# Performance work log

Measured on AMD Instinct MI355X. Metric: run time of the kernel, lower is better.

The kernel has to match this reference:

```python
import jax, jax.numpy as jnp
import numpy as np

BRANCH = 8
LEVELS = 7
N = (BRANCH ** LEVELS - 1) // (BRANCH - 1)  # 299593 nodes, complete 8-ary tree
VOCAB, IN_DIM, MEM = 50000, 300, 150


def _tree_structure():
    parent = np.empty(N, np.int32)
    parent[0] = N  # sentinel: root scatters into dropped segment N
    idx = np.arange(1, N)
    parent[1:] = (idx - 1) // BRANCH
    depth = np.empty(N, np.int32)
    start = 0
    for d in range(LEVELS):
        cnt = BRANCH ** d
        depth[start:start + cnt] = d
        start += cnt
    return jnp.asarray(parent), jnp.asarray(depth)


def setup_inputs() -> dict:
    key = jax.random.key(0)
    ks = jax.random.split(key, 20)
    parent, depth = _tree_structure()
    inp = {
        'tokens': jax.random.randint(ks[0], (N,), 0, VOCAB, dtype=jnp.int32),
        'parent': parent,
        'depth': depth,
        'max_depth': LEVELS,
        'emb': jax.random.normal(ks[1], (VOCAB, IN_DIM), jnp.float32) * 0.1,
    }
    names_x = ['Wix', 'Wfx', 'Wox', 'Wux']
    names_h = ['Wih', 'Wfh', 'Woh', 'Wuh']
    sx = 1.0 / np.sqrt(IN_DIM)
    sh = 1.0 / np.sqrt(MEM)
    for j, (nx, nh) in enumerate(zip(names_x, names_h)):
        inp[nx] = jax.random.normal(ks[2 + 4 * j], (MEM, IN_DIM), jnp.float32) * sx
        inp['b' + nx[1:]] = jax.random.normal(ks[3 + 4 * j], (MEM,), jnp.float32) * sx
        inp[nh] = jax.random.normal(ks[4 + 4 * j], (MEM, MEM), jnp.float32) * sh
        inp['b' + nh[1:]] = jax.random.normal(ks[5 + 4 * j], (MEM,), jnp.float32) * sh
    return inp


def reference(tokens, parent, depth, max_depth, emb,
              Wix, bix, Wih, bih, Wfx, bfx, Wfh, bfh,
              Wox, box, Woh, boh, Wux, bux, Wuh, buh):
    n = tokens.shape[0]
    x = emb[tokens]  # [N, in_dim]
    # precompute all input-side gate projections once (batched GEMMs)
    ix_x = x @ Wix.T + bix
    fx_x = x @ Wfx.T + bfx
    ox_x = x @ Wox.T + box
    ux_x = x @ Wux.T + bux
    # parent index safe for gathering (root's sentinel -> 0; its row is masked out)
    gparent = jnp.where(parent >= n, 0, parent)

    h = jnp.zeros((n, MEM), x.dtype)
    c = jnp.zeros((n, MEM), x.dtype)

    # level-synchronous bottom-up sweep (loop over tree depth, not data)
    for d in range(max_depth - 1, -1, -1):
        # per-child forget gate: sigmoid(fh(h_child) + fx(x_parent)) * c_child
        f = jax.nn.sigmoid(h @ Wfh.T + bfh + fx_x[gparent])
        fc_sum = jax.ops.segment_sum(f * c, parent, num_segments=n + 1)[:n]
        h_sum = jax.ops.segment_sum(h, parent, num_segments=n + 1)[:n]
        i = jax.nn.sigmoid(ix_x + h_sum @ Wih.T + bih)
        o = jax.nn.sigmoid(ox_x + h_sum @ Woh.T + boh)
        u = jnp.tanh(ux_x + h_sum @ Wuh.T + buh)
        c_new = i * u + fc_sum
        h_new = o * jnp.tanh(c_new)
        mask = (depth == d)[:, None]
        c = jnp.where(mask, c_new, c)
        h = jnp.where(mask, h_new, h)
    # original returns concatenated cell states (post-order); here indexed by node id
    return c
```

## Files before the change

kernel.cpp:

```cpp
#include <hip/hip_runtime.h>


#define MEMD  150
#define IND   300
#define NINT  37449
#define VOCAB 50000
#define XROW  608
#define FSTR  152
#define NVB   1563
#define NNB   1171

typedef short bf16x8 __attribute__((ext_vector_type(8)));
typedef float f32x16 __attribute__((ext_vector_type(16)));
#define ZERO16 {0,0,0,0,0,0,0,0,0,0,0,0,0,0,0,0}

#define XINT_OFF 0ul
#define HLF_OFF  45540000ul
#define FHX_OFF  60740000ul
#define HSB_OFF  68340000ul
#define FCS_OFF  79730000ul
#define BPX_OFF  91120000ul
#define BPH_OFF  91510000ul

#define CLF_OUT_OFF 0ul

__device__ __forceinline__ float b2f(unsigned short u) {
    union { unsigned int i; float f; } v; v.i = ((unsigned int)u) << 16; return v.f;
}
__device__ __forceinline__ unsigned short f2b(float f) {
    union { float f; unsigned int i; } v; v.f = f;
    unsigned int x = v.i;
    x += 0x7fffu + ((x >> 16) & 1u);
    return (unsigned short)(x >> 16);
}
__device__ __forceinline__ float sigm(float x) {
    return __builtin_amdgcn_rcpf(1.0f + __expf(-x));
}
__device__ __forceinline__ float tanh_fast(float x) {
    float e = __expf(2.0f * x);
    return 1.0f - 2.0f * __builtin_amdgcn_rcpf(e + 1.0f);
}
__device__ __forceinline__ unsigned char f2e4m3(float f) {
    union { float f; unsigned u; } v; v.f = f;
    unsigned s = (v.u >> 31) << 7;
    float af = fabsf(f);
    if (af >= 448.f) return (unsigned char)(s | 0x7E);
    if (af < 0.015625f) {
        int m = (int)(af * 512.f + 0.5f);
        if (m > 7) m = 7;
        return (unsigned char)(s | m);
    }
    unsigned u = v.u & 0x7fffffffu;
    u += 0x7ffffu + ((u >> 20) & 1u);
    int ef = (int)(u >> 23) - 120;
    unsigned m = (u >> 20) & 7u;
    if (ef < 1) { ef = 1; m = 0; }
    if (ef > 15) { ef = 15; m = 6; }
    return (unsigned char)(s | (ef << 3) | m);
}
__device__ __forceinline__ float e4m3f(unsigned char u) {
    unsigned s = (u >> 7) & 1u, ef = (u >> 3) & 15u, m = u & 7u;
    if (ef == 0) {
        float r = (float)m * 0.001953125f;
        return s ? -r : r;
    }
    union { unsigned u; float f; } v;
    v.u = (s << 31) | ((ef + 120) << 23) | (m << 20);
    return v.f;
}

__global__ void pack_w(const float* __restrict__ Wix, const float* __restrict__ Wox,
                       const float* __restrict__ Wux, const float* __restrict__ Wfx,
                       const float* __restrict__ Wih, const float* __restrict__ Woh,
                       const float* __restrict__ Wuh, const float* __restrict__ Wfh,
                       unsigned short* __restrict__ bpx, unsigned short* __restrict__ bph)
{
    const int total_x = 4 * 5 * 19 * 512;
    const int total_h = 4 * 5 * 10 * 512;
    for (int i = blockIdx.x * blockDim.x + threadIdx.x; i < total_x + total_h;
         i += gridDim.x * blockDim.x) {
        if (i < total_x) {
            int e = i & 7, lane = (i >> 3) & 63, rest = i >> 9;
            int ks = rest % 19; rest /= 19;
            int nt = rest % 5;  int g = rest / 5;
            int col = nt * 32 + (lane & 31);
            int k = ks * 16 + ((lane >> 5) << 3) + e;
            const float* W = (g == 0) ? Wix : (g == 1) ? Wox : (g == 2) ? Wux : Wfx;
            bpx[i] = f2b((col < MEMD && k < IND) ? W[col * IND + k] : 0.f);
        } else {
            int j = i - total_x;
            int e = j & 7, lane = (j >> 3) & 63, rest = j >> 9;
            int ks = rest % 10; rest /= 10;
            int nt = rest % 5;  int g = rest / 5;
            int col = nt * 32 + (lane & 31);
            int k = ks * 16 + ((lane >> 5) << 3) + e;
            const float* W = (g == 0) ? Wih : (g == 1) ? Woh : (g == 2) ? Wuh : Wfh;
            bph[j] = f2b((col < MEMD && k < MEMD) ? W[col * MEMD + k] : 0.f);
        }
    }
}

__global__ __launch_bounds__(320, 3)
void xgemm_all(const int* __restrict__ tokens, const float* __restrict__ emb,
               const float* __restrict__ bix, const float* __restrict__ bih,
               const float* __restrict__ box_, const float* __restrict__ boh,
               const float* __restrict__ bux, const float* __restrict__ buh,
               const float* __restrict__ bfx, const float* __restrict__ bfh,
               const unsigned short* __restrict__ bpx_u,
               const unsigned short* __restrict__ bph_u,
               unsigned short* __restrict__ cleaf,
               unsigned short* __restrict__ hleaf,
               unsigned char* __restrict__ fhx,
               unsigned short* __restrict__ xint)
{
    __shared__ __align__(16) char sm0[32768];
    __shared__ int toksL[32];
    const int tid = threadIdx.x, lane = tid & 63, w = tid >> 6;
    const int hi = lane >> 5, ln31 = lane & 31;
    const bool isV = blockIdx.x < NVB;
    const int tile0 = (isV ? blockIdx.x : (blockIdx.x - NVB)) * 32;
    const int rowsValid = min(32, (isV ? VOCAB : NINT) - tile0);

    if (tid < 32) {
        int rr = (tid < rowsValid) ? tid : 0;
        toksL[tid] = isV ? (tile0 + rr) : tokens[tile0 + rr];
    }
    __syncthreads();
    for (int i = tid; i < 32 * 40; i += 320) {
        int r = i / 40, q = i % 40;
        const float* er = emb + (long)toksL[r] * IND;
        float4 v0 = {0.f,0.f,0.f,0.f}, v1 = {0.f,0.f,0.f,0.f};
        if (q < 38) v0 = *(const float4*)(er + q * 8);
        if (q < 37) v1 = *(const float4*)(er + q * 8 + 4);
        bf16x8 p;
        p[0]=(short)f2b(v0.x); p[1]=(short)f2b(v0.y); p[2]=(short)f2b(v0.z); p[3]=(short)f2b(v0.w);
        p[4]=(short)f2b(v1.x); p[5]=(short)f2b(v1.y); p[6]=(short)f2b(v1.z); p[7]=(short)f2b(v1.w);
        *(bf16x8*)(sm0 + r * 640 + ((q * 16) ^ ((r & 7) << 4))) = p;
    }
    __syncthreads();

    const bf16x8* BX = (const bf16x8*)bpx_u;
    const bf16x8* BH = (const bf16x8*)bph_u;
    const int row = ln31, nt = w;
    const int col = nt * 32 + ln31;
    const bool colv = col < MEMD;
    const int cc = colv ? col : 0;

    f32x16 a0 = ZERO16, a1 = ZERO16, a2 = ZERO16, a3 = ZERO16;
    {
        bf16x8 aC = *(const bf16x8*)(sm0 + row * 640 + ((hi * 16) ^ ((row & 7) << 4)));
        bf16x8 b0C = BX[((0 * 5 + nt) * 19 + 0) * 64 + lane];
        bf16x8 b1C = BX[((1 * 5 + nt) * 19 + 0) * 64 + lane];
        bf16x8 b2C = BX[((2 * 5 + nt) * 19 + 0) * 64 + lane];
        bf16x8 b3C = BX[((3 * 5 + nt) * 19 + 0) * 64 + lane];
        #pragma unroll
        for (int ks = 0; ks < 19; ++ks) {
            bf16x8 aN, b0N, b1N, b2N, b3N;
            if (ks < 18) {
                aN  = *(const bf16x8*)(sm0 + row * 640 + (((ks + 1) * 32 + hi * 16) ^ ((row & 7) << 4)));
                b0N = BX[((0 * 5 + nt) * 19 + ks + 1) * 64 + lane];
                b1N = BX[((1 * 5 + nt) * 19 + ks + 1) * 64 + lane];
                b2N = BX[((2 * 5 + nt) * 19 + ks + 1) * 64 + lane];
                if (!isV) b3N = BX[((3 * 5 + nt) * 19 + ks + 1) * 64 + lane];
            }
            a0 = __builtin_amdgcn_mfma_f32_32x32x16_bf16(aC, b0C, a0, 0, 0, 0);
            a1 = __builtin_amdgcn_mfma_f32_32x32x16_bf16(aC, b1C, a1, 0, 0, 0);
            a2 = __builtin_amdgcn_mfma_f32_32x32x16_bf16(aC, b2C, a2, 0, 0, 0);
            if (!isV) a3 = __builtin_amdgcn_mfma_f32_32x32x16_bf16(aC, b3C, a3, 0, 0, 0);
            aC = aN; b0C = b0N; b1C = b1N; b2C = b2N; b3C = b3N;
        }
    }
    const float bi = bix[cc] + bih[cc];
    const float bo = box_[cc] + boh[cc];
    const float bu = bux[cc] + buh[cc];

    if (isV) {
        #pragma unroll
        for (int r = 0; r < 16; ++r) {
            int rloc = (r & 3) + 8 * (r >> 2) + 4 * hi;
            float iv = sigm(a0[r] + bi);
            float ov = sigm(a1[r] + bo);
            float uv = tanh_fast(a2[r] + bu);
            float cv = iv * uv;
            float hv = ov * tanh_fast(cv);
            if (rloc < rowsValid && colv) {
                long o = (long)(tile0 + rloc) * FSTR + col;
                cleaf[o] = f2b(cv);
                hleaf[o] = f2b(hv);
            }
            *(unsigned short*)(sm0 + 20480 + rloc * 384 + ((col * 2) ^ ((rloc & 7) << 4))) = f2b(hv);
        }
        __syncthreads();
        f32x16 ff = ZERO16;
        {
            const char* hb = sm0 + 20480;
            bf16x8 aC = *(const bf16x8*)(hb + row * 384 + ((hi * 16) ^ ((row & 7) << 4)));
            bf16x8 bC = BH[((15 + nt) * 10 + 0) * 64 + lane];
            #pragma unroll
            for (int ks = 0; ks < 10; ++ks) {
                bf16x8 aN, bN;
                if (ks < 9) {
                    aN = *(const bf16x8*)(hb + row * 384 + (((ks + 1) * 32 + hi * 16) ^ ((row & 7) << 4)));
                    bN = BH[((15 + nt) * 10 + ks + 1) * 64 + lane];
                }
                ff = __builtin_amdgcn_mfma_f32_32x32x16_bf16(aC, bC, ff, 0, 0, 0);
                aC = aN; bC = bN;
            }
        }
        if (colv) {
            #pragma unroll
            for (int r = 0; r < 16; ++r) {
                int rloc = (r & 3) + 8 * (r >> 2) + 4 * hi;
                if (rloc < rowsValid)
                    fhx[(long)(tile0 + rloc) * FSTR + col] = f2e4m3(ff[r]);
            }
        }
    } else {
        const float bf = bfx[cc] + bfh[cc];
        #pragma unroll
        for (int r = 0; r < 16; ++r) {
            int rloc = (r & 3) + 8 * (r >> 2) + 4 * hi;
            if (rloc < rowsValid && colv) {
                ushort4 gv;
                gv.x = f2b(a0[r] + bi);
                gv.y = f2b(a1[r] + bo);
                gv.z = f2b(a2[r] + bu);
                gv.w = f2b(a3[r] + bf);
                *(ushort4*)(xint + (long)(tile0 + rloc) * XROW + col * 4) = gv;
            }
        }
    }
}

__global__ __launch_bounds__(320, 8)
void leaf_csum(const int* __restrict__ tokens,
               const unsigned short* __restrict__ cleafU,
               const unsigned short* __restrict__ hleaf,
               const unsigned char* __restrict__ fhx,
               const unsigned short* __restrict__ xint,
               unsigned short* __restrict__ hsumb, unsigned short* __restrict__ fcs,
               float* __restrict__ c_out)
{
    __shared__ int ctok[16];
    const int tid = threadIdx.x;
    const int pl = tid / 160;
    const int col0 = tid % 160;
    const bool colv = col0 < MEMD;
    const int col = colv ? col0 : (MEMD - 1);
    const int pnode = 4681 + blockIdx.x * 2 + pl;
    const long cbase = 8L * pnode + 1;
    if (tid < 16) ctok[tid] = tokens[37449 + blockIdx.x * 16 + tid];
    __syncthreads();

    const float fxp = b2f(xint[(long)pnode * XROW + col * 4 + 3]);
    float hs = 0.f, fc = 0.f;
    #pragma unroll
    for (int k = 0; k < 8; ++k) {
        int ct = ctok[pl * 8 + k];
        long o = (long)ct * FSTR + col;
        float cv = b2f(cleafU[o]);
        float h  = b2f(hleaf[o]);
        float f  = sigm(e4m3f(fhx[o]) + fxp);
        hs += h;
        fc += f * cv;
        if (colv) c_out[(cbase + k) * MEMD + col] = cv;
    }
    if (colv) {
        hsumb[(long)pnode * FSTR + col] = f2b(hs);
        fcs[(long)pnode * FSTR + col]  = f2b(fc);
    }
}

__global__ __launch_bounds__(320, 2)
void level_k(const unsigned short* __restrict__ xint,
             const unsigned short* __restrict__ bph_u,
             unsigned short* __restrict__ hsumb, unsigned short* __restrict__ fcsum,
             float* __restrict__ c_out, int base, int cnt, int writePar)
{
    __shared__ __align__(16) char sm0[24576];
    const int tid = threadIdx.x, lane = tid & 63, w = tid >> 6;
    const int hi = lane >> 5, ln31 = lane & 31;
    const int tile0 = blockIdx.x * 32;
    const int nodeBase = base + tile0;
    const int rowsValid = min(32, cnt - tile0);
    const int p0 = (nodeBase - 1) >> 3;
    const int nt = w;

    for (int i = tid; i < 32 * 20; i += 320) {
        int r = i / 20, q = i % 20;
        int rr = (r < rowsValid) ? r : 0;
        bf16x8 v = {0,0,0,0,0,0,0,0};
        if (q < 19)
            v = *(const bf16x8*)(hsumb + (long)(nodeBase + rr) * FSTR + q * 8);
        *(bf16x8*)(sm0 + 12288 + r * 384 + ((q * 16) ^ ((r & 7) << 4))) = v;
    }
    __syncthreads();

    const bf16x8* BH = (const bf16x8*)bph_u;
    const int row = ln31;
    const int col = nt * 32 + ln31;
    const bool colv = col < MEMD;
    const int cc = colv ? col : 0;

    f32x16 ai = ZERO16, ao = ZERO16, au = ZERO16;
    {
        const char* hb = sm0 + 12288;
        bf16x8 aC = *(const bf16x8*)(hb + row * 384 + ((hi * 16) ^ ((row & 7) << 4)));
        bf16x8 b0C = BH[((0 * 5 + nt) * 10 + 0) * 64 + lane];
        bf16x8 b1C = BH[((1 * 5 + nt) * 10 + 0) * 64 + lane];
        bf16x8 b2C = BH[((2 * 5 + nt) * 10 + 0) * 64 + lane];
        #pragma unroll
        for (int ks = 0; ks < 10; ++ks) {
            bf16x8 aN, b0N, b1N, b2N;
            if (ks < 9) {
                aN  = *(const bf16x8*)(hb + row * 384 + (((ks + 1) * 32 + hi * 16) ^ ((row & 7) << 4)));
                b0N = BH[((0 * 5 + nt) * 10 + ks + 1) * 64 + lane];
                b1N = BH[((1 * 5 + nt) * 10 + ks + 1) * 64 + lane];
                b2N = BH[((2 * 5 + nt) * 10 + ks + 1) * 64 + lane];
            }
            ai = __builtin_amdgcn_mfma_f32_32x32x16_bf16(aC, b0C, ai, 0, 0, 0);
            ao = __builtin_amdgcn_mfma_f32_32x32x16_bf16(aC, b1C, ao, 0, 0, 0);
            au = __builtin_amdgcn_mfma_f32_32x32x16_bf16(aC, b2C, au, 0, 0, 0);
            aC = aN; b0C = b0N; b1C = b1N; b2C = b2N;
        }
    }

    float cvv[16];
    {
        float hp[4] = {0.f, 0.f, 0.f, 0.f};
        #pragma unroll
        for (int r = 0; r < 16; ++r) {
            int rloc = (r & 3) + 8 * (r >> 2) + 4 * hi;
            bool rv = rloc < rowsValid;
            int rr = rv ? rloc : 0;
            ushort4 gv = *(const ushort4*)(xint + (long)(nodeBase + rr) * XROW + cc * 4);
            float fcin = (rv && colv) ? b2f(fcsum[(long)(nodeBase + rloc) * FSTR + col]) : 0.f;
            float iv = sigm(ai[r] + b2f(gv.x));
            float ov = sigm(ao[r] + b2f(gv.y));
            float uv = tanh_fast(au[r] + b2f(gv.z));
            float cv = iv * uv + fcin;
            float h = (rv && colv) ? ov * tanh_fast(cv) : 0.f;
            cvv[r] = (rv && colv) ? cv : 0.f;
            if (rv && colv) c_out[(long)(nodeBase + rloc) * MEMD + col] = cv;
            *(unsigned short*)(sm0 + rloc * 384 + ((col * 2) ^ ((rloc & 7) << 4))) = f2b(h);
            hp[r >> 2] += h;
        }
        if (writePar) {
            #pragma unroll
            for (int o = 0; o < 4; ++o) {
                float s = hp[o] + __shfl_xor(hp[o], 32);
                if (lane < 32 && colv && o * 8 < rowsValid)
                    hsumb[(long)(p0 + o) * FSTR + col] = f2b(s);
            }
        }
    }
    __syncthreads();

    if (writePar) {
        f32x16 ff = ZERO16;
        {
            bf16x8 aC = *(const bf16x8*)(sm0 + row * 384 + ((hi * 16) ^ ((row & 7) << 4)));
            bf16x8 bC = BH[((15 + nt) * 10 + 0) * 64 + lane];
            #pragma unroll
            for (int ks = 0; ks < 10; ++ks) {
                bf16x8 aN, bN;
                if (ks < 9) {
                    aN = *(const bf16x8*)(sm0 + row * 384 + (((ks + 1) * 32 + hi * 16) ^ ((row & 7) << 4)));
                    bN = BH[((15 + nt) * 10 + ks + 1) * 64 + lane];
                }
                ff = __builtin_amdgcn_mfma_f32_32x32x16_bf16(aC, bC, ff, 0, 0, 0);
                aC = aN; bC = bN;
            }
        }
        #pragma unroll
        for (int o = 0; o < 4; ++o) {
            float fx = b2f(xint[(long)(p0 + o) * XROW + cc * 4 + 3]);
            float fp = 0.f;
            #pragma unroll
            for (int q = 0; q < 4; ++q) {
                int r = o * 4 + q;
                fp += sigm(ff[r] + fx) * cvv[r];
            }
            float s = fp + __shfl_xor(fp, 32);
            if (lane < 32 && colv && o * 8 < rowsValid)
                fcsum[(long)(p0 + o) * FSTR + col] = f2b(s);
        }
    }
}

__global__ __launch_bounds__(320, 2)
void tail_k(const unsigned short* __restrict__ xint,
            const unsigned short* __restrict__ bph_u,
            unsigned short* __restrict__ hsumb, unsigned short* __restrict__ fcsum,
            float* __restrict__ c_out)
{
    __shared__ __align__(16) char sm0[24576];
    const int tid = threadIdx.x, lane = tid & 63, w = tid >> 6;
    const int hi = lane >> 5, ln31 = lane & 31;
    const int nt = w;
    const bf16x8* BH = (const bf16x8*)bph_u;
    const int row = ln31;
    const int col = nt * 32 + ln31;
    const bool colv = col < MEMD;
    const int cc = colv ? col : 0;

    const int basesL[3] = {9, 1, 0};
    const int cntsL[3]  = {64, 8, 1};
    const int wpL[3]    = {1, 1, 0};

    for (int li = 0; li < 3; ++li) {
        for (int t0 = 0; t0 < cntsL[li]; t0 += 32) {
            const int nb = basesL[li] + t0;
            const int rv32 = min(32, cntsL[li] - t0);
            const int pp0 = (nb - 1) >> 3;
            const int writePar = wpL[li];

            for (int i = tid; i < 32 * 20; i += 320) {
                int r = i / 20, q = i % 20;
                int rr = (r < rv32) ? r : 0;
                bf16x8 v = {0,0,0,0,0,0,0,0};
                if (q < 19)
                    v = *(const bf16x8*)(hsumb + (long)(nb + rr) * FSTR + q * 8);
                *(bf16x8*)(sm0 + 12288 + r * 384 + ((q * 16) ^ ((r & 7) << 4))) = v;
            }
            __syncthreads();

            f32x16 ai = ZERO16, ao = ZERO16, au = ZERO16;
            {
                const char* hb = sm0 + 12288;
                #pragma unroll
                for (int ks = 0; ks < 10; ++ks) {
                    bf16x8 a = *(const bf16x8*)(hb + row * 384 + ((ks * 32 + hi * 16) ^ ((row & 7) << 4)));
                    ai = __builtin_amdgcn_mfma_f32_32x32x16_bf16(a, BH[((0 * 5 + nt) * 10 + ks) * 64 + lane], ai, 0, 0, 0);
                    ao = __builtin_amdgcn_mfma_f32_32x32x16_bf16(a, BH[((1 * 5 + nt) * 10 + ks) * 64 + lane], ao, 0, 0, 0);
                    au = __builtin_amdgcn_mfma_f32_32x32x16_bf16(a, BH[((2 * 5 + nt) * 10 + ks) * 64 + lane], au, 0, 0, 0);
                }
            }

            float cvv[16];
            {
                float hp[4] = {0.f, 0.f, 0.f, 0.f};
                #pragma unroll
                for (int r = 0; r < 16; ++r) {
                    int rloc = (r & 3) + 8 * (r >> 2) + 4 * hi;
                    bool rv = rloc < rv32;
                    int rr = rv ? rloc : 0;
                    ushort4 gv = *(const ushort4*)(xint + (long)(nb + rr) * XROW + cc * 4);
                    float fcin = (rv && colv) ? b2f(fcsum[(long)(nb + rloc) * FSTR + col]) : 0.f;
                    float iv = sigm(ai[r] + b2f(gv.x));
                    float ov = sigm(ao[r] + b2f(gv.y));
                    float uv = tanh_fast(au[r] + b2f(gv.z));
                    float cv = iv * uv + fcin;
                    float h = (rv && colv) ? ov * tanh_fast(cv) : 0.f;
                    cvv[r] = (rv && colv) ? cv : 0.f;
                    if (rv && colv) c_out[(long)(nb + rloc) * MEMD + col] = cv;
                    *(unsigned short*)(sm0 + rloc * 384 + ((col * 2) ^ ((rloc & 7) << 4))) = f2b(h);
                    hp[r >> 2] += h;
                }
                if (writePar) {
                    #pragma unroll
                    for (int o = 0; o < 4; ++o) {
                        float s = hp[o] + __shfl_xor(hp[o], 32);
                        if (lane < 32 && colv && o * 8 < rv32)
                            hsumb[(long)(pp0 + o) * FSTR + col] = f2b(s);
                    }
                }
            }
            __syncthreads();

            if (writePar) {
                f32x16 ff = ZERO16;
                #pragma unroll
                for (int ks = 0; ks < 10; ++ks) {
                    bf16x8 a = *(const bf16x8*)(sm0 + row * 384 + ((ks * 32 + hi * 16) ^ ((row & 7) << 4)));
                    ff = __builtin_amdgcn_mfma_f32_32x32x16_bf16(a, BH[((15 + nt) * 10 + ks) * 64 + lane], ff, 0, 0, 0);
                }
                #pragma unroll
                for (int o = 0; o < 4; ++o) {
                    float fx = b2f(xint[(long)(pp0 + o) * XROW + cc * 4 + 3]);
                    float fp = 0.f;
                    #pragma unroll
                    for (int q = 0; q < 4; ++q)
                        fp += sigm(ff[o * 4 + q] + fx) * cvv[o * 4 + q];
                    float s = fp + __shfl_xor(fp, 32);
                    if (lane < 32 && colv && o * 8 < rv32)
                        fcsum[(long)(pp0 + o) * FSTR + col] = f2b(s);
                }
            }
            __syncthreads();
        }
    }
}

extern "C" void kernel_launch(void* const* d_in, const int* in_sizes, int n_in,
                              void* d_out, int out_size, void* d_ws, size_t ws_size,
                              hipStream_t stream) {
    const int*   tokens = (const int*)d_in[0];
    const float* emb = (const float*)d_in[4];
    const float* Wix = (const float*)d_in[5];  const float* bix = (const float*)d_in[6];
    const float* Wih = (const float*)d_in[7];  const float* bih = (const float*)d_in[8];
    const float* Wfx = (const float*)d_in[9];  const float* bfx = (const float*)d_in[10];
    const float* Wfh = (const float*)d_in[11]; const float* bfh = (const float*)d_in[12];
    const float* Wox = (const float*)d_in[13]; const float* box_ = (const float*)d_in[14];
    const float* Woh = (const float*)d_in[15]; const float* boh = (const float*)d_in[16];
    const float* Wux = (const float*)d_in[17]; const float* bux = (const float*)d_in[18];
    const float* Wuh = (const float*)d_in[19]; const float* buh = (const float*)d_in[20];
    float* c_out = (float*)d_out;
    char* ws = (char*)d_ws;
    char* outb = (char*)d_out;

    unsigned short* xint  = (unsigned short*)(ws + XINT_OFF);
    unsigned short* hleaf = (unsigned short*)(ws + HLF_OFF);
    unsigned char*  fhx   = (unsigned char*)(ws + FHX_OFF);
    unsigned short* hsumb = (unsigned short*)(ws + HSB_OFF);
    unsigned short* fcs   = (unsigned short*)(ws + FCS_OFF);
    unsigned short* bpx   = (unsigned short*)(ws + BPX_OFF);
    unsigned short* bph   = (unsigned short*)(ws + BPH_OFF);
    unsigned short* cleafU = (unsigned short*)(outb + CLF_OUT_OFF);

    pack_w<<<128, 512, 0, stream>>>(Wix, Wox, Wux, Wfx, Wih, Woh, Wuh, Wfh, bpx, bph);
    xgemm_all<<<NVB + NNB, 320, 0, stream>>>(
        tokens, emb, bix, bih, box_, boh, bux, buh, bfx, bfh,
        bpx, bph, cleafU, hleaf, fhx, xint);
    leaf_csum<<<16384, 320, 0, stream>>>(tokens, cleafU, hleaf, fhx, xint, hsumb, fcs, c_out);

    static const int bases[3] = {4681, 585, 73};
    static const int cnts[3]  = {32768, 4096, 512};
    for (int d = 0; d < 3; ++d) {
        int grid = (cnts[d] + 31) / 32;
        level_k<<<grid, 320, 0, stream>>>(
            xint, bph, hsumb, fcs, c_out, bases[d], cnts[d], 1);
    }
    tail_k<<<1, 320, 0, stream>>>(xint, bph, hsumb, fcs, c_out);
}
```

Before: 280.8 us.

## Process 64-row tiles in the input-projection GEMM to reuse weight fragments

Doubles the row tile of the fused embedding/input-projection kernel from 32 to 64 rows, so each weight fragment loaded from global memory feeds two MFMAs (one per 32-row half). This halves the block count and the weight traffic per row. The internal-node path splits its four gate GEMMs into two passes of two gates each, which keeps register pressure down, and writes the outputs as paired ushort2 stores. The explicit software prefetch of the next k-step is dropped and LDS use grows to 40 KB, which may lower occupancy and latency hiding on this small GEMM.

```diff
diff --git a/kernel.cpp b/kernel.cpp
--- a/kernel.cpp
+++ b/kernel.cpp
@@ -7,8 +7,8 @@
 #define VOCAB 50000
 #define XROW  608
 #define FSTR  152
-#define NVB   1563
-#define NNB   1171
+#define NVB64 782
+#define NNB64 586
 
 typedef short bf16x8 __attribute__((ext_vector_type(8)));
 typedef float f32x16 __attribute__((ext_vector_type(16)));
@@ -101,32 +101,32 @@
 }
 
 __global__ __launch_bounds__(320, 3)
-void xgemm_all(const int* __restrict__ tokens, const float* __restrict__ emb,
-               const float* __restrict__ bix, const float* __restrict__ bih,
-               const float* __restrict__ box_, const float* __restrict__ boh,
-               const float* __restrict__ bux, const float* __restrict__ buh,
-               const float* __restrict__ bfx, const float* __restrict__ bfh,
-               const unsigned short* __restrict__ bpx_u,
-               const unsigned short* __restrict__ bph_u,
-               unsigned short* __restrict__ cleaf,
-               unsigned short* __restrict__ hleaf,
-               unsigned char* __restrict__ fhx,
-               unsigned short* __restrict__ xint)
+void xgemm64(const int* __restrict__ tokens, const float* __restrict__ emb,
+             const float* __restrict__ bix, const float* __restrict__ bih,
+             const float* __restrict__ box_, const float* __restrict__ boh,
+             const float* __restrict__ bux, const float* __restrict__ buh,
+             const float* __restrict__ bfx, const float* __restrict__ bfh,
+             const unsigned short* __restrict__ bpx_u,
+             const unsigned short* __restrict__ bph_u,
+             unsigned short* __restrict__ cleaf,
+             unsigned short* __restrict__ hleaf,
+             unsigned char* __restrict__ fhx,
+             unsigned short* __restrict__ xint)
 {
-    __shared__ __align__(16) char sm0[32768];
-    __shared__ int toksL[32];
+    __shared__ __align__(16) char sm0[40960];
+    __shared__ int toksL[64];
     const int tid = threadIdx.x, lane = tid & 63, w = tid >> 6;
     const int hi = lane >> 5, ln31 = lane & 31;
-    const bool isV = blockIdx.x < NVB;
-    const int tile0 = (isV ? blockIdx.x : (blockIdx.x - NVB)) * 32;
-    const int rowsValid = min(32, (isV ? VOCAB : NINT) - tile0);
-
-    if (tid < 32) {
+    const bool isV = blockIdx.x < NVB64;
+    const int tile0 = (isV ? blockIdx.x : (blockIdx.x - NVB64)) * 64;
+    const int rowsValid = min(64, (isV ? VOCAB : NINT) - tile0);
+
+    if (tid < 64) {
         int rr = (tid < rowsValid) ? tid : 0;
         toksL[tid] = isV ? (tile0 + rr) : tokens[tile0 + rr];
     }
     __syncthreads();
-    for (int i = tid; i < 32 * 40; i += 320) {
+    for (int i = tid; i < 64 * 40; i += 320) {
         int r = i / 40, q = i % 40;
         const float* er = emb + (long)toksL[r] * IND;
         float4 v0 = {0.f,0.f,0.f,0.f}, v1 = {0.f,0.f,0.f,0.f};
@@ -141,95 +141,148 @@
 
     const bf16x8* BX = (const bf16x8*)bpx_u;
     const bf16x8* BH = (const bf16x8*)bph_u;
-    const int row = ln31, nt = w;
+    const int nt = w;
     const int col = nt * 32 + ln31;
     const bool colv = col < MEMD;
     const int cc = colv ? col : 0;
-
-    f32x16 a0 = ZERO16, a1 = ZERO16, a2 = ZERO16, a3 = ZERO16;
-    {
-        bf16x8 aC = *(const bf16x8*)(sm0 + row * 640 + ((hi * 16) ^ ((row & 7) << 4)));
-        bf16x8 b0C = BX[((0 * 5 + nt) * 19 + 0) * 64 + lane];
-        bf16x8 b1C = BX[((1 * 5 + nt) * 19 + 0) * 64 + lane];
-        bf16x8 b2C = BX[((2 * 5 + nt) * 19 + 0) * 64 + lane];
-        bf16x8 b3C = BX[((3 * 5 + nt) * 19 + 0) * 64 + lane];
+    const int r0 = ln31, r1 = 32 + ln31;
+
+#define LDA(rr, ks) (*(const bf16x8*)(sm0 + (rr) * 640 + (((ks) * 32 + hi * 16) ^ (((rr) & 7) << 4))))
+
+    if (isV) {
+        f32x16 ai0 = ZERO16, ai1 = ZERO16, ao0 = ZERO16, ao1 = ZERO16,
+               au0 = ZERO16, au1 = ZERO16;
         #pragma unroll
         for (int ks = 0; ks < 19; ++ks) {
-            bf16x8 aN, b0N, b1N, b2N, b3N;
-            if (ks < 18) {
-                aN  = *(const bf16x8*)(sm0 + row * 640 + (((ks + 1) * 32 + hi * 16) ^ ((row & 7) << 4)));
-                b0N = BX[((0 * 5 + nt) * 19 + ks + 1) * 64 + lane];
-                b1N = BX[((1 * 5 + nt) * 19 + ks + 1) * 64 + lane];
-                b2N = BX[((2 * 5 + nt) * 19 + ks + 1) * 64 + lane];
-                if (!isV) b3N = BX[((3 * 5 + nt) * 19 + ks + 1) * 64 + lane];
-            }
-            a0 = __builtin_amdgcn_mfma_f32_32x32x16_bf16(aC, b0C, a0, 0, 0, 0);
-            a1 = __builtin_amdgcn_mfma_f32_32x32x16_bf16(aC, b1C, a1, 0, 0, 0);
-            a2 = __builtin_amdgcn_mfma_f32_32x32x16_bf16(aC, b2C, a2, 0, 0, 0);
-            if (!isV) a3 = __builtin_amdgcn_mfma_f32_32x32x16_bf16(aC, b3C, a3, 0, 0, 0);
-            aC = aN; b0C = b0N; b1C = b1N; b2C = b2N; b3C = b3N;
-        }
-    }
-    const float bi = bix[cc] + bih[cc];
-    const float bo = box_[cc] + boh[cc];
-    const float bu = bux[cc] + buh[cc];
-
-    if (isV) {
+            bf16x8 a0 = LDA(r0, ks);
+            bf16x8 a1 = LDA(r1, ks);
+            bf16x8 b0 = BX[((0 * 5 + nt) * 19 + ks) * 64 + lane];
+            bf16x8 b1 = BX[((1 * 5 + nt) * 19 + ks) * 64 + lane];
+            bf16x8 b2 = BX[((2 * 5 + nt) * 19 + ks) * 64 + lane];
+            ai0 = __builtin_amdgcn_mfma_f32_32x32x16_bf16(a0, b0, ai0, 0, 0, 0);
+            ai1 = __builtin_amdgcn_mfma_f32_32x32x16_bf16(a1, b0, ai1, 0, 0, 0);
+            ao0 = __builtin_amdgcn_mfma_f32_32x32x16_bf16(a0, b1, ao0, 0, 0, 0);
+            ao1 = __builtin_amdgcn_mfma_f32_32x32x16_bf16(a1, b1, ao1, 0, 0, 0);
+            au0 = __builtin_amdgcn_mfma_f32_32x32x16_bf16(a0, b2, au0, 0, 0, 0);
+            au1 = __builtin_amdgcn_mfma_f32_32x32x16_bf16(a1, b2, au1, 0, 0, 0);
+        }
+        const float bi = bix[cc] + bih[cc];
+        const float bo = box_[cc] + boh[cc];
+        const float bu = bux[cc] + buh[cc];
+        float hv0[16], hv1[16];
         #pragma unroll
         for (int r = 0; r < 16; ++r) {
-            int rloc = (r & 3) + 8 * (r >> 2) + 4 * hi;
-            float iv = sigm(a0[r] + bi);
-            float ov = sigm(a1[r] + bo);
-            float uv = tanh_fast(a2[r] + bu);
-            float cv = iv * uv;
-            float hv = ov * tanh_fast(cv);
-            if (rloc < rowsValid && colv) {
-                long o = (long)(tile0 + rloc) * FSTR + col;
-                cleaf[o] = f2b(cv);
-                hleaf[o] = f2b(hv);
-            }
-            *(unsigned short*)(sm0 + 20480 + rloc * 384 + ((col * 2) ^ ((rloc & 7) << 4))) = f2b(hv);
+            int rl = (r & 3) + 8 * (r >> 2) + 4 * hi;
+            float iv = sigm(ai0[r] + bi), ov = sigm(ao0[r] + bo), uv = tanh_fast(au0[r] + bu);
+            float cv = iv * uv; float hv = ov * tanh_fast(cv);
+            hv0[r] = hv;
+            if (rl < rowsValid && colv) {
+                long o = (long)(tile0 + rl) * FSTR + col;
+                cleaf[o] = f2b(cv); hleaf[o] = f2b(hv);
+            }
+            int rl1 = 32 + rl;
+            iv = sigm(ai1[r] + bi); ov = sigm(ao1[r] + bo); uv = tanh_fast(au1[r] + bu);
+            cv = iv * uv; hv = ov * tanh_fast(cv);
+            hv1[r] = hv;
+            if (rl1 < rowsValid && colv) {
+                long o = (long)(tile0 + rl1) * FSTR + col;
+                cleaf[o] = f2b(cv); hleaf[o] = f2b(hv);
+            }
         }
         __syncthreads();
-        f32x16 ff = ZERO16;
-        {
-            const char* hb = sm0 + 20480;
-            bf16x8 aC = *(const bf16x8*)(hb + row * 384 + ((hi * 16) ^ ((row & 7) << 4)));
-            bf16x8 bC = BH[((15 + nt) * 10 + 0) * 64 + lane];
-            #pragma unroll
-            for (int ks = 0; ks < 10; ++ks) {
-                bf16x8 aN, bN;
-                if (ks < 9) {
-                    aN = *(const bf16x8*)(hb + row * 384 + (((ks + 1) * 32 + hi * 16) ^ ((row & 7) << 4)));
-                    bN = BH[((15 + nt) * 10 + ks + 1) * 64 + lane];
-                }
-                ff = __builtin_amdgcn_mfma_f32_32x32x16_bf16(aC, bC, ff, 0, 0, 0);
-                aC = aN; bC = bN;
-            }
+        #pragma unroll
+        for (int r = 0; r < 16; ++r) {
+            int rl = (r & 3) + 8 * (r >> 2) + 4 * hi;
+            *(unsigned short*)(sm0 + rl * 384 + ((col * 2) ^ ((rl & 7) << 4))) = f2b(hv0[r]);
+            int rl1 = 32 + rl;
+            *(unsigned short*)(sm0 + rl1 * 384 + ((col * 2) ^ ((rl1 & 7) << 4))) = f2b(hv1[r]);
+        }
+        __syncthreads();
+        f32x16 f0 = ZERO16, f1 = ZERO16;
+        #pragma unroll
+        for (int ks = 0; ks < 10; ++ks) {
+            bf16x8 a0 = *(const bf16x8*)(sm0 + r0 * 384 + ((ks * 32 + hi * 16) ^ ((r0 & 7) << 4)));
+            bf16x8 a1 = *(const bf16x8*)(sm0 + r1 * 384 + ((ks * 32 + hi * 16) ^ ((r1 & 7) << 4)));
+            bf16x8 b = BH[((15 + nt) * 10 + ks) * 64 + lane];
+            f0 = __builtin_amdgcn_mfma_f32_32x32x16_bf16(a0, b, f0, 0, 0, 0);
+            f1 = __builtin_amdgcn_mfma_f32_32x32x16_bf16(a1, b, f1, 0, 0, 0);
         }
         if (colv) {
             #pragma unroll
             for (int r = 0; r < 16; ++r) {
-                int rloc = (r & 3) + 8 * (r >> 2) + 4 * hi;
-                if (rloc < rowsValid)
-                    fhx[(long)(tile0 + rloc) * FSTR + col] = f2e4m3(ff[r]);
+                int rl = (r & 3) + 8 * (r >> 2) + 4 * hi;
+                if (rl < rowsValid)
+                    fhx[(long)(tile0 + rl) * FSTR + col] = f2e4m3(f0[r]);
+                int rl1 = 32 + rl;
+                if (rl1 < rowsValid)
+                    fhx[(long)(tile0 + rl1) * FSTR + col] = f2e4m3(f1[r]);
             }
         }
     } else {
-        const float bf = bfx[cc] + bfh[cc];
-        #pragma unroll
-        for (int r = 0; r < 16; ++r) {
-            int rloc = (r & 3) + 8 * (r >> 2) + 4 * hi;
-            if (rloc < rowsValid && colv) {
-                ushort4 gv;
-                gv.x = f2b(a0[r] + bi);
-                gv.y = f2b(a1[r] + bo);
-                gv.z = f2b(a2[r] + bu);
-                gv.w = f2b(a3[r] + bf);
-                *(ushort4*)(xint + (long)(tile0 + rloc) * XROW + col * 4) = gv;
-            }
-        }
-    }
+        {
+            f32x16 p00 = ZERO16, p01 = ZERO16, p10 = ZERO16, p11 = ZERO16;
+            #pragma unroll
+            for (int ks = 0; ks < 19; ++ks) {
+                bf16x8 a0 = LDA(r0, ks);
+                bf16x8 a1 = LDA(r1, ks);
+                bf16x8 b0 = BX[((0 * 5 + nt) * 19 + ks) * 64 + lane];
+                bf16x8 b1 = BX[((1 * 5 + nt) * 19 + ks) * 64 + lane];
+                p00 = __builtin_amdgcn_mfma_f32_32x32x16_bf16(a0, b0, p00, 0, 0, 0);
+                p01 = __builtin_amdgcn_mfma_f32_32x32x16_bf16(a1, b0, p01, 0, 0, 0);
+                p10 = __builtin_amdgcn_mfma_f32_32x32x16_bf16(a0, b1, p10, 0, 0, 0);
+                p11 = __builtin_amdgcn_mfma_f32_32x32x16_bf16(a1, b1, p11, 0, 0, 0);
+            }
+            const float bi = bix[cc] + bih[cc];
+            const float bo = box_[cc] + boh[cc];
+            if (colv) {
+                #pragma unroll
+                for (int r = 0; r < 16; ++r) {
+                    int rl = (r & 3) + 8 * (r >> 2) + 4 * hi;
+                    if (rl < rowsValid) {
+                        ushort2 v; v.x = f2b(p00[r] + bi); v.y = f2b(p10[r] + bo);
+                        *(ushort2*)(xint + (long)(tile0 + rl) * XROW + col * 4) = v;
+                    }
+                    int rl1 = 32 + rl;
+                    if (rl1 < rowsValid) {
+                        ushort2 v; v.x = f2b(p01[r] + bi); v.y = f2b(p11[r] + bo);
+                        *(ushort2*)(xint + (long)(tile0 + rl1) * XROW + col * 4) = v;
+                    }
+                }
+            }
+        }
+        {
+            f32x16 p00 = ZERO16, p01 = ZERO16, p10 = ZERO16, p11 = ZERO16;
+            #pragma unroll
+            for (int ks = 0; ks < 19; ++ks) {
+                bf16x8 a0 = LDA(r0, ks);
+                bf16x8 a1 = LDA(r1, ks);
+                bf16x8 b0 = BX[((2 * 5 + nt) * 19 + ks) * 64 + lane];
+                bf16x8 b1 = BX[((3 * 5 + nt) * 19 + ks) * 64 + lane];
+                p00 = __builtin_amdgcn_mfma_f32_32x32x16_bf16(a0, b0, p00, 0, 0, 0);
+                p01 = __builtin_amdgcn_mfma_f32_32x32x16_bf16(a1, b0, p01, 0, 0, 0);
+                p10 = __builtin_amdgcn_mfma_f32_32x32x16_bf16(a0, b1, p10, 0, 0, 0);
+                p11 = __builtin_amdgcn_mfma_f32_32x32x16_bf16(a1, b1, p11, 0, 0, 0);
+            }
+            const float bu = bux[cc] + buh[cc];
+            const float bf = bfx[cc] + bfh[cc];
+            if (colv) {
+                #pragma unroll
+                for (int r = 0; r < 16; ++r) {
+                    int rl = (r & 3) + 8 * (r >> 2) + 4 * hi;
+                    if (rl < rowsValid) {
+                        ushort2 v; v.x = f2b(p00[r] + bu); v.y = f2b(p10[r] + bf);
+                        *(ushort2*)(xint + (long)(tile0 + rl) * XROW + col * 4 + 2) = v;
+                    }
+                    int rl1 = 32 + rl;
+                    if (rl1 < rowsValid) {
+                        ushort2 v; v.x = f2b(p01[r] + bu); v.y = f2b(p11[r] + bf);
+                        *(ushort2*)(xint + (long)(tile0 + rl1) * XROW + col * 4 + 2) = v;
+                    }
+                }
+            }
+        }
+    }
+#undef LDA
 }
 
 __global__ __launch_bounds__(320, 8)
@@ -519,7 +572,7 @@
     unsigned short* cleafU = (unsigned short*)(outb + CLF_OUT_OFF);
 
     pack_w<<<128, 512, 0, stream>>>(Wix, Wox, Wux, Wfx, Wih, Woh, Wuh, Wfh, bpx, bph);
-    xgemm_all<<<NVB + NNB, 320, 0, stream>>>(
+    xgemm64<<<NVB64 + NNB64, 320, 0, stream>>>(
         tokens, emb, bix, bih, box_, boh, bux, buh, bfx, bfh,
         bpx, bph, cleafU, hleaf, fhx, xint);
     leaf_csum<<<16384, 320, 0, stream>>>(tokens, cleafU, hleaf, fhx, xint, hsumb, fcs, c_out);
```

New measurement: 330.9 us. +17.9%, slower.
